# Kernel optimization log

Measured on AMD Instinct MI355X. Metric: run time of the kernel, lower is better.

## Reference

```python
import jax, jax.numpy as jnp
import numpy as np

N, C, K, H = 131072, 256, 32, 8      # points, dim, patch_size, heads
NW = N // K                           # number of windows (4096)
POS_BND = int(0.8 * K)                # 25, as in OctFormer RPE (dilation=1)
RPE_NUM = 2 * POS_BND + 1             # 51


def layer_norm(x, g, b, eps=1e-5):
    m = x.mean(-1, keepdims=True)
    v = jnp.var(x, axis=-1, keepdims=True)
    return (x - m) * jax.lax.rsqrt(v + eps) * g + b


def setup_inputs() -> dict:
    key = jax.random.key(0)
    ks = jax.random.split(key, 12)
    s = 0.02
    return dict(
        data=jax.random.normal(ks[0], (N, C), jnp.float32),
        nbr_idx=jax.random.randint(ks[1], (N, 27), 0, N, dtype=jnp.int32),
        rel_pos=(jax.random.randint(ks[2], (NW, K, K, 3), 0, 2 * K + 1, dtype=jnp.int32) - K),
        patch_mask=jnp.zeros((NW, K, K), jnp.float32),
        w_cpe=jax.random.normal(ks[3], (27, C), jnp.float32) * s,
        bn_g=jnp.ones((C,), jnp.float32), bn_b=jnp.zeros((C,), jnp.float32),
        n1_g=jnp.ones((C,), jnp.float32), n1_b=jnp.zeros((C,), jnp.float32),
        w_qkv=jax.random.normal(ks[4], (C, 3 * C), jnp.float32) * s,
        b_qkv=jnp.zeros((3 * C,), jnp.float32),
        w_proj=jax.random.normal(ks[5], (C, C), jnp.float32) * s,
        b_proj=jnp.zeros((C,), jnp.float32),
        rpe_table=jax.random.normal(ks[6], (3 * RPE_NUM, H), jnp.float32) * s,
        n2_g=jnp.ones((C,), jnp.float32), n2_b=jnp.zeros((C,), jnp.float32),
        w_fc1=jax.random.normal(ks[7], (C, 4 * C), jnp.float32) * s,
        b_fc1=jnp.zeros((4 * C,), jnp.float32),
        w_fc2=jax.random.normal(ks[8], (4 * C, C), jnp.float32) * s,
        b_fc2=jnp.zeros((C,), jnp.float32),
    )


def reference(data, nbr_idx, rel_pos, patch_mask, w_cpe, bn_g, bn_b,
              n1_g, n1_b, w_qkv, b_qkv, w_proj, b_proj, rpe_table,
              n2_g, n2_b, w_fc1, b_fc1, w_fc2, b_fc2):
    # CPE: depthwise 27-neighbor octree conv + eval-mode batchnorm affine
    cpe = jnp.einsum('njc,jc->nc', data[nbr_idx], w_cpe)  # [N,27,C] gather
    data = data + (cpe * bn_g + bn_b)
    # data_to_windows: [N,C] -> [NW,K,C] (N divisible by K)
    x = data.reshape(NW, K, C)

    # windowed attention with inline RPE + additive patch mask
    h = layer_norm(x, n1_g, n1_b)
    qkv = (h @ w_qkv + b_qkv).reshape(NW, K, 3, H, C // H)
    q, k, v = qkv[:, :, 0], qkv[:, :, 1], qkv[:, :, 2]
    scale = (C // H) ** -0.5
    attn = jnp.einsum('nqhd,nkhd->nhqk', q * scale, k)     # [NW,H,K,K]
    idx = jnp.clip(rel_pos, -POS_BND, POS_BND) + POS_BND + jnp.arange(3) * RPE_NUM
    rpe = rpe_table[idx].sum(3)                             # [NW,K,K,H]
    attn = attn + rpe.transpose(0, 3, 1, 2) + patch_mask[:, None]
    attn = jax.nn.softmax(attn, axis=-1)
    out = jnp.einsum('nhqk,nkhd->nqhd', attn, v).reshape(NW, K, C)
    x = x + (out @ w_proj + b_proj)                         # gamma1 = 1

    # MLP (GELU, exact erf like torch default)
    h2 = layer_norm(x, n2_g, n2_b)
    x = x + (jax.nn.gelu(h2 @ w_fc1 + b_fc1, approximate=False) @ w_fc2 + b_fc2)
    return x.reshape(N, C)
```

## Files before the change

kernel.cpp:

```cpp
#include <hip/hip_runtime.h>
#include <stdint.h>


static constexpr int NPT   = 131072;
static constexpr int CC    = 256;
static constexpr int NWIN  = 4096;
static constexpr int NHEAD = 8;

using u16 = unsigned short;
using u32 = unsigned int;
using u8  = unsigned char;

typedef __bf16 bf16x8 __attribute__((ext_vector_type(8)));
typedef float  f32x4  __attribute__((ext_vector_type(4)));
typedef u32    u32x4  __attribute__((ext_vector_type(4)));
typedef u32    u32x2  __attribute__((ext_vector_type(2)));

__device__ __forceinline__ float b2f(u16 u) {
  union { float f; u32 i; } v; v.i = ((u32)u) << 16; return v.f;
}
__device__ __forceinline__ u16 f2b(float f) {
  u32 x = __float_as_uint(f);
  return (u16)((x + 0x7fffu + ((x >> 16) & 1u)) >> 16);
}

__device__ __forceinline__ u8 f2fp8(float f) {
  const u32 s = (__float_as_uint(f) >> 24) & 0x80u;
  float a = fabsf(f);
  if (a >= 0.015625f) {
    u32 b = __float_as_uint(a);
    u32 rb = b + 0x7FFFFu + ((b >> 20) & 1u);
    u32 E = (rb >> 23) - 120u;
    return (u8)(s | (E << 3) | ((rb >> 20) & 7u));
  }
  int k = (int)rintf(a * 512.0f);
  return (u8)(s | (u32)k);
}

template <int J>
__device__ __forceinline__ float fp82f(u32 d) {
#if defined(__has_builtin)
#if __has_builtin(__builtin_amdgcn_cvt_f32_fp8)
  return __builtin_amdgcn_cvt_f32_fp8(d, J);
#else
  const u32 u = (d >> (8 * J)) & 0xFFu;
  const u32 e = (u >> 3) & 15u, m = u & 7u;
  float v = e ? __uint_as_float(((e + 120u) << 23) | (m << 20))
              : (float)m * 0.001953125f;
  return (u & 0x80u) ? -v : v;
#endif
#else
  const u32 u = (d >> (8 * J)) & 0xFFu;
  const u32 e = (u >> 3) & 15u, m = u & 7u;
  float v = e ? __uint_as_float(((e + 120u) << 23) | (m << 20))
              : (float)m * 0.001953125f;
  return (u & 0x80u) ? -v : v;
#endif
}

__device__ __forceinline__ void gload_lds16(const void* g, void* l) {
  using gptr_t = const __attribute__((address_space(1))) uint32_t*;
  using lptr_t = __attribute__((address_space(3))) uint32_t*;
  __builtin_amdgcn_global_load_lds((gptr_t)(uintptr_t)g,
                                   (lptr_t)(uint32_t)(uintptr_t)l, 16, 0, 0);
}

__global__ __launch_bounds__(256) void k_f2b8(const float* __restrict__ in,
                                              u8* __restrict__ out, int n4) {
  for (int i = blockIdx.x * 256 + threadIdx.x; i < n4; i += gridDim.x * 256) {
    float4 v = ((const float4*)in)[i];
    u32 o = (u32)f2fp8(v.x) | ((u32)f2fp8(v.y) << 8) |
            ((u32)f2fp8(v.z) << 16) | ((u32)f2fp8(v.w) << 24);
    ((u32*)out)[i] = o;
  }
}

__global__ __launch_bounds__(256) void k_prep_w(
    const float* __restrict__ wqkv, const float* __restrict__ wproj,
    const float* __restrict__ wfc1, const float* __restrict__ wfc2,
    u16* __restrict__ oqkv, u16* __restrict__ oproj,
    u16* __restrict__ ofc1, u16* __restrict__ ofc2) {
  int i = blockIdx.x * 256 + threadIdx.x;
  if (i < 196608) {
    int c = i >> 8, r = i & 255; oqkv[i] = f2b(wqkv[r * 768 + c]);
  } else if (i < 262144) {
    i -= 196608; int c = i >> 8, r = i & 255; oproj[i] = f2b(wproj[r * 256 + c]);
  } else if (i < 524288) {
    i -= 262144; int c = i >> 8, r = i & 255; ofc1[i] = f2b(wfc1[r * 1024 + c]);
  } else {
    i -= 524288; int c = i >> 10, r = i & 1023; ofc2[i] = f2b(wfc2[r * 256 + c]);
  }
}

__global__ __launch_bounds__(256) void k_cpe_ln1(
    const float* __restrict__ data, const int* __restrict__ nbr,
    const u8* __restrict__ datab, const float* __restrict__ w_cpe,
    const float* __restrict__ bn_g, const float* __restrict__ bn_b,
    const float* __restrict__ n1_g, const float* __restrict__ n1_b,
    float* __restrict__ xo, u16* __restrict__ ho) {
  const int wv   = threadIdx.x >> 6;
  const int lane = threadIdx.x & 63;
  const int n    = blockIdx.x * 4 + wv;
  const int c0   = lane * 4;

  int myidx = 0;
  if (lane < 27) myidx = nbr[n * 27 + lane];

  u32 d[27];
#pragma unroll
  for (int j = 0; j < 27; j++) {
    const int idx = __builtin_amdgcn_readlane(myidx, j);
    d[j] = *(const u32*)(datab + (size_t)idx * CC + c0);
  }

  float a0 = 0.f, a1 = 0.f, a2 = 0.f, a3 = 0.f;
#pragma unroll
  for (int j = 0; j < 27; j++) {
    const float4 wj = *(const float4*)(w_cpe + j * CC + c0);
    a0 += fp82f<0>(d[j]) * wj.x;
    a1 += fp82f<1>(d[j]) * wj.y;
    a2 += fp82f<2>(d[j]) * wj.z;
    a3 += fp82f<3>(d[j]) * wj.w;
  }

  const float4 dv = *(const float4*)(data + (size_t)n * CC + c0);
  const float4 g4 = *(const float4*)(bn_g + c0);
  const float4 b4 = *(const float4*)(bn_b + c0);
  float x0 = dv.x + a0 * g4.x + b4.x;
  float x1 = dv.y + a1 * g4.y + b4.y;
  float x2 = dv.z + a2 * g4.z + b4.z;
  float x3 = dv.w + a3 * g4.w + b4.w;
  *(float4*)(xo + (size_t)n * CC + c0) = make_float4(x0, x1, x2, x3);

  float s  = x0 + x1 + x2 + x3;
  float s2 = x0 * x0 + x1 * x1 + x2 * x2 + x3 * x3;
#pragma unroll
  for (int m = 1; m <= 32; m <<= 1) { s += __shfl_xor(s, m); s2 += __shfl_xor(s2, m); }
  const float mean = s * (1.f / 256.f);
  const float var  = s2 * (1.f / 256.f) - mean * mean;
  const float inv  = rsqrtf(var + 1e-5f);

  const float4 ng = *(const float4*)(n1_g + c0);
  const float4 nb4 = *(const float4*)(n1_b + c0);
  u32x2 o;
  o[0] = (u32)f2b((x0 - mean) * inv * ng.x + nb4.x) |
         ((u32)f2b((x1 - mean) * inv * ng.y + nb4.y) << 16);
  o[1] = (u32)f2b((x2 - mean) * inv * ng.z + nb4.z) |
         ((u32)f2b((x3 - mean) * inv * ng.w + nb4.w) << 16);
  *(u32x2*)(ho + (size_t)n * CC + c0) = o;
}

template <int KD, int ND, int EPI>
__global__ __launch_bounds__(256) void k_gemm(const u16* __restrict__ A,
                                              const u16* __restrict__ Bt,
                                              const float* __restrict__ bias,
                                              u16* __restrict__ outb,
                                              float* __restrict__ outf) {
  __shared__ __align__(16) u16 As[128 * 64];
  __shared__ __align__(16) u16 Bs[128 * 64];
  const int tid = threadIdx.x;
  const int lane = tid & 63;
  const int wv = tid >> 6;
  const int wm = (wv >> 1) * 64;
  const int wn = (wv & 1) * 64;
  const int l15 = lane & 15;
  const int lhi = lane >> 4;

  const int gx = gridDim.x;
  const int bid = blockIdx.y * gx + blockIdx.x;
  const int cpx = (gx * gridDim.y) >> 3;
  const int swz = (bid & 7) * cpx + (bid >> 3);
  const int m0 = (swz / gx) * 128;
  const int n0 = (swz % gx) * 128;

  f32x4 acc[4][4] = {};

  for (int k0 = 0; k0 < KD; k0 += 64) {
#pragma unroll
    for (int i = 0; i < 4; i++) {
      const int off = i * 4096 + tid * 16;
      const int row = off >> 7;
      const int ke  = (off & 127) >> 1;
      gload_lds16(A  + (size_t)(m0 + row) * KD + k0 + ke, (char*)As + off);
      gload_lds16(Bt + (size_t)(n0 + row) * KD + k0 + ke, (char*)Bs + off);
    }
    __syncthreads();
#pragma unroll
    for (int kk = 0; kk < 2; kk++) {
      bf16x8 fa[4], fb[4];
#pragma unroll
      for (int t = 0; t < 4; t++) {
        fa[t] = *(const bf16x8*)&As[(wm + t * 16 + l15) * 64 + kk * 32 + lhi * 8];
        fb[t] = *(const bf16x8*)&Bs[(wn + t * 16 + l15) * 64 + kk * 32 + lhi * 8];
      }
#pragma unroll
      for (int mi = 0; mi < 4; mi++)
#pragma unroll
        for (int ni = 0; ni < 4; ni++)
          acc[mi][ni] = __builtin_amdgcn_mfma_f32_16x16x32_bf16(fa[mi], fb[ni],
                                                                acc[mi][ni], 0, 0, 0);
    }
    __syncthreads();
  }

#pragma unroll
  for (int mi = 0; mi < 4; mi++) {
#pragma unroll
    for (int ni = 0; ni < 4; ni++) {
      const int col = n0 + wn + ni * 16 + l15;
      const float bc = bias[col];
#pragma unroll
      for (int r = 0; r < 4; r++) {
        const int row = m0 + wm + mi * 16 + lhi * 4 + r;
        const size_t o = (size_t)row * ND + col;
        float v = acc[mi][ni][r] + bc;
        if constexpr (EPI == 0) {
          outb[o] = f2b(v);
        } else if constexpr (EPI == 1) {
          outf[o] += v;
        } else {
          v = 0.5f * v * (1.0f + erff(v * 0.70710678118654752f));
          outb[o] = f2b(v);
        }
      }
    }
  }
}

__global__ __launch_bounds__(256) void k_proj_ln2(
    const u16* __restrict__ A, const u16* __restrict__ Bt,
    const float* __restrict__ bias, float* __restrict__ xo,
    const float* __restrict__ n2g, const float* __restrict__ n2b,
    u16* __restrict__ h2) {
  __shared__ __align__(16) u16 As[128 * 64];
  __shared__ __align__(16) u16 Bs[256 * 64];
  const int tid = threadIdx.x;
  const int lane = tid & 63;
  const int wv = tid >> 6;
  const int l15 = lane & 15;
  const int g = lane >> 4;
  const int m0 = blockIdx.x * 128;
  const int wm = wv * 32;

  f32x4 acc[2][16] = {};

  for (int k0 = 0; k0 < 256; k0 += 64) {
#pragma unroll
    for (int i = 0; i < 4; i++) {
      const int off = i * 4096 + tid * 16;
      const int row = off >> 7, ke = (off & 127) >> 1;
      gload_lds16(A + (size_t)(m0 + row) * 256 + k0 + ke, (char*)As + off);
    }
#pragma unroll
    for (int i = 0; i < 8; i++) {
      const int off = i * 4096 + tid * 16;
      const int row = off >> 7, ke = (off & 127) >> 1;
      gload_lds16(Bt + (size_t)row * 256 + k0 + ke, (char*)Bs + off);
    }
    __syncthreads();
#pragma unroll
    for (int kk = 0; kk < 2; kk++) {
      bf16x8 fa[2];
#pragma unroll
      for (int t = 0; t < 2; t++)
        fa[t] = *(const bf16x8*)&As[(wm + t * 16 + l15) * 64 + kk * 32 + g * 8];
#pragma unroll
      for (int ni = 0; ni < 16; ni++) {
        bf16x8 fb = *(const bf16x8*)&Bs[(ni * 16 + l15) * 64 + kk * 32 + g * 8];
#pragma unroll
        for (int mi = 0; mi < 2; mi++)
          acc[mi][ni] = __builtin_amdgcn_mfma_f32_16x16x32_bf16(fa[mi], fb,
                                                                acc[mi][ni], 0, 0, 0);
      }
    }
    __syncthreads();
  }

#pragma unroll
  for (int mi = 0; mi < 2; mi++) {
#pragma unroll
    for (int r = 0; r < 4; r++) {
      const int row = m0 + wm + mi * 16 + g * 4 + r;
      float v[16];
      float s = 0.f, s2 = 0.f;
#pragma unroll
      for (int ni = 0; ni < 16; ni++) {
        const int col = ni * 16 + l15;
        float t = acc[mi][ni][r] + bias[col] + xo[(size_t)row * 256 + col];
        v[ni] = t; s += t; s2 += t * t;
      }
#pragma unroll
      for (int m = 1; m <= 8; m <<= 1) { s += __shfl_xor(s, m); s2 += __shfl_xor(s2, m); }
      const float mean = s * (1.f / 256.f);
      const float var  = s2 * (1.f / 256.f) - mean * mean;
      const float inv  = rsqrtf(var + 1e-5f);
#pragma unroll
      for (int ni = 0; ni < 16; ni++) {
        const int col = ni * 16 + l15;
        xo[(size_t)row * 256 + col] = v[ni];
        h2[(size_t)row * 256 + col] = f2b((v[ni] - mean) * inv * n2g[col] + n2b[col]);
      }
    }
  }
}

__global__ __launch_bounds__(512, 4) void k_attn(const u16* __restrict__ qkv,
                                                 const int* __restrict__ rel_pos,
                                                 const float* __restrict__ pmask,
                                                 const float* __restrict__ rpet,
                                                 u16* __restrict__ out) {
  constexpr int HS = 1288;
  __shared__ __align__(16) u16 smem[24 * HS + 2448];
  u16* sQ = smem;
  u16* sK = smem + 8 * HS;
  u16* sV = smem + 16 * HS;
  float* sT = (float*)(smem + 24 * HS);

  const int tid = threadIdx.x;
  const int nw  = blockIdx.x;
  const int w32 = nw * 32;

  for (int i = tid; i < 1224; i += 512) {
    int h = i / 153, ix = i - h * 153;
    sT[i] = rpet[ix * 8 + h];
  }
#pragma unroll
  for (int j = 0; j < 4; j++) {
    int id  = j * 512 + tid;
    int mat = id >> 10;
    int id1 = id & 1023;
    int h = id1 >> 7, q = (id1 >> 2) & 31, s = id1 & 3;
    u32x4 v = *(const u32x4*)(qkv + (size_t)(w32 + q) * 768 + mat * 256 + h * 32 + s * 8);
    u16* dst = (mat ? sK : sQ) + h * HS + q * 40 + s * 8;
    *(u32x4*)dst = v;
  }
#pragma unroll
  for (int j = 0; j < 2; j++) {
    int id = j * 512 + tid;
    int p = id >> 5, dc = id & 31;
    u32x4 v = *(const u32x4*)(qkv + (size_t)(w32 + p) * 768 + 512 + dc * 8);
    const u16* pv = (const u16*)&v;
#pragma unroll
    for (int jj = 0; jj < 8; jj++) {
      int d = dc * 8 + jj;
      sV[(d >> 5) * HS + (d & 31) * 40 + p] = pv[jj];
    }
  }
  __syncthreads();

  const int h = tid >> 6;
  const int lane = tid & 63;
  const int g = lane >> 4, c = lane & 15;
  const f32x4 zero = {0.f, 0.f, 0.f, 0.f};

  bf16x8 fq[2], fk[2];
#pragma unroll
  for (int t = 0; t < 2; t++) {
    fq[t] = *(const bf16x8*)&sQ[h * HS + (t * 16 + c) * 40 + g * 8];
    fk[t] = *(const bf16x8*)&sK[h * HS + (t * 16 + c) * 40 + g * 8];
  }
  f32x4 S[2][2];
#pragma unroll
  for (int qt = 0; qt < 2; qt++)
#pragma unroll
    for (int kt = 0; kt < 2; kt++)
      S[qt][kt] = __builtin_amdgcn_mfma_f32_16x16x32_bf16(fq[qt], fk[kt], zero, 0, 0, 0);

  const float sc = 0.17677669529663687f;
#pragma unroll
  for (int qt = 0; qt < 2; qt++) {
#pragma unroll
    for (int r = 0; r < 4; r++) {
      const int q = qt * 16 + g * 4 + r;
      const int* rp = rel_pos + ((size_t)(w32 + q) * 32) * 3;
      const float* pm = pmask + (size_t)(w32 + q) * 32;
      float v[2];
#pragma unroll
      for (int kt = 0; kt < 2; kt++) {
        const int k = kt * 16 + c;
        int r0 = rp[k * 3], r1 = rp[k * 3 + 1], r2 = rp[k * 3 + 2];
        r0 = min(max(r0, -25), 25);
        r1 = min(max(r1, -25), 25);
        r2 = min(max(r2, -25), 25);
        const float b = sT[h * 153 + 25 + r0] + sT[h * 153 + 76 + r1] +
                        sT[h * 153 + 127 + r2] + pm[k];
        v[kt] = S[qt][kt][r] * sc + b;
      }
      float m = fmaxf(v[0], v[1]);
#pragma unroll
      for (int d = 1; d <= 8; d <<= 1) m = fmaxf(m, __shfl_xor(m, d));
      const float e0 = __expf(v[0] - m);
      const float e1 = __expf(v[1] - m);
      float ssum = e0 + e1;
#pragma unroll
      for (int d = 1; d <= 8; d <<= 1) ssum += __shfl_xor(ssum, d);
      const float inv = 1.0f / ssum;
      sQ[h * HS + q * 40 + c]      = f2b(e0 * inv);
      sQ[h * HS + q * 40 + 16 + c] = f2b(e1 * inv);
    }
  }
  __builtin_amdgcn_sched_barrier(0);

  bf16x8 fp[2], fv[2];
#pragma unroll
  for (int t = 0; t < 2; t++) {
    fp[t] = *(const bf16x8*)&sQ[h * HS + (t * 16 + c) * 40 + g * 8];
    fv[t] = *(const bf16x8*)&sV[h * HS + (t * 16 + c) * 40 + g * 8];
  }
  f32x4 OT[2][2];
#pragma unroll
  for (int dt = 0; dt < 2; dt++)
#pragma unroll
    for (int qt = 0; qt < 2; qt++)
      OT[dt][qt] = __builtin_amdgcn_mfma_f32_16x16x32_bf16(fv[dt], fp[qt], zero, 0, 0, 0);

  __syncthreads();
  u16* OL = sK;
#pragma unroll
  for (int dt = 0; dt < 2; dt++)
#pragma unroll
    for (int qt = 0; qt < 2; qt++)
#pragma unroll
      for (int r = 0; r < 4; r++) {
        const int d = dt * 16 + g * 4 + r, q = qt * 16 + c;
        OL[q * 264 + h * 32 + d] = f2b(OT[dt][qt][r]);
      }
  __syncthreads();

  {
    const int q = tid >> 4, ch = tid & 15;
    u32x4 w0 = *(const u32x4*)&OL[q * 264 + ch * 16];
    u32x4 w1 = *(const u32x4*)&OL[q * 264 + ch * 16 + 8];
    u16* ob = out + (size_t)(w32 + q) * 256 + ch * 16;
    *(u32x4*)ob = w0;
    *((u32x4*)ob + 1) = w1;
  }
}

extern "C" void kernel_launch(void* const* d_in, const int* in_sizes, int n_in,
                              void* d_out, int out_size, void* d_ws, size_t ws_size,
                              hipStream_t stream) {
  const float* data   = (const float*)d_in[0];
  const int*   nbr    = (const int*)d_in[1];
  const int*   relpos = (const int*)d_in[2];
  const float* pmask  = (const float*)d_in[3];
  const float* w_cpe  = (const float*)d_in[4];
  const float* bn_g   = (const float*)d_in[5];
  const float* bn_b   = (const float*)d_in[6];
  const float* n1_g   = (const float*)d_in[7];
  const float* n1_b   = (const float*)d_in[8];
  const float* w_qkv  = (const float*)d_in[9];
  const float* b_qkv  = (const float*)d_in[10];
  const float* w_proj = (const float*)d_in[11];
  const float* b_proj = (const float*)d_in[12];
  const float* rpet   = (const float*)d_in[13];
  const float* n2_g   = (const float*)d_in[14];
  const float* n2_b   = (const float*)d_in[15];
  const float* w_fc1  = (const float*)d_in[16];
  const float* b_fc1  = (const float*)d_in[17];
  const float* w_fc2  = (const float*)d_in[18];
  const float* b_fc2  = (const float*)d_in[19];
  float* xout = (float*)d_out;

  char* pw = (char*)d_ws;
  u16* buf1 = (u16*)pw; pw += (size_t)NPT * 1024 * 2;
  u16* buf2 = (u16*)pw; pw += (size_t)NPT * 256 * 2;
  u16* wqkvT = (u16*)pw; pw += 768 * 256 * 2;
  u16* wprojT = (u16*)pw; pw += 256 * 256 * 2;
  u16* wfc1T = (u16*)pw; pw += 1024 * 256 * 2;
  u16* wfc2T = (u16*)pw; pw += 256 * 1024 * 2;
  u8* data8 = (u8*)buf1;

  k_f2b8<<<2048, 256, 0, stream>>>(data, data8, NPT * 256 / 4);
  k_prep_w<<<3072, 256, 0, stream>>>(w_qkv, w_proj, w_fc1, w_fc2,
                                     wqkvT, wprojT, wfc1T, wfc2T);

  k_cpe_ln1<<<NPT / 4, 256, 0, stream>>>(data, nbr, data8, w_cpe, bn_g, bn_b, n1_g, n1_b,
                                         xout, buf2);
  k_gemm<256, 768, 0><<<dim3(6, 1024), 256, 0, stream>>>(buf2, wqkvT, b_qkv, buf1, nullptr);
  k_attn<<<NWIN, 512, 0, stream>>>(buf1, relpos, pmask, rpet, buf2);
  k_proj_ln2<<<1024, 256, 0, stream>>>(buf2, wprojT, b_proj, xout, n2_g, n2_b, buf2);
  k_gemm<256, 1024, 2><<<dim3(8, 1024), 256, 0, stream>>>(buf2, wfc1T, b_fc1, buf1, nullptr);
  k_gemm<1024, 256, 1><<<dim3(2, 1024), 256, 0, stream>>>(buf1, wfc2T, b_fc2, nullptr, xout);
}
```

Baseline: 916.3 us.

## Run FC2 GEMM in FP8 and stage CPE weights in shared memory

The FC1 epilogue now writes the GELU activations as FP8 instead of bf16, FC2 weights are converted to FP8, and a new FP8 MFMA GEMM kernel computes FC2. This halves the bytes moved for the largest intermediate and uses the faster FP8 matrix instructions. The CPE/LN1 kernel also loads the depthwise weights into LDS once per block and processes 16 points per block instead of 4, which cuts repeated global weight reads. Both FP8 steps lower the precision of the MLP path.

```diff
diff --git a/kernel.cpp b/kernel.cpp
--- a/kernel.cpp
+++ b/kernel.cpp
@@ -79,7 +79,7 @@
     const float* __restrict__ wqkv, const float* __restrict__ wproj,
     const float* __restrict__ wfc1, const float* __restrict__ wfc2,
     u16* __restrict__ oqkv, u16* __restrict__ oproj,
-    u16* __restrict__ ofc1, u16* __restrict__ ofc2) {
+    u16* __restrict__ ofc1, u8* __restrict__ ofc2) {
   int i = blockIdx.x * 256 + threadIdx.x;
   if (i < 196608) {
     int c = i >> 8, r = i & 255; oqkv[i] = f2b(wqkv[r * 768 + c]);
@@ -88,7 +88,7 @@
   } else if (i < 524288) {
     i -= 262144; int c = i >> 8, r = i & 255; ofc1[i] = f2b(wfc1[r * 1024 + c]);
   } else {
-    i -= 524288; int c = i >> 10, r = i & 1023; ofc2[i] = f2b(wfc2[r * 256 + c]);
+    i -= 524288; int c = i >> 10, r = i & 1023; ofc2[i] = f2fp8(wfc2[r * 256 + c]);
   }
 }
 
@@ -98,56 +98,74 @@
     const float* __restrict__ bn_g, const float* __restrict__ bn_b,
     const float* __restrict__ n1_g, const float* __restrict__ n1_b,
     float* __restrict__ xo, u16* __restrict__ ho) {
-  const int wv   = threadIdx.x >> 6;
-  const int lane = threadIdx.x & 63;
-  const int n    = blockIdx.x * 4 + wv;
+  __shared__ __align__(16) float sW[27 * 256];
+  const int tid = threadIdx.x;
+  {
+    const float4* src = (const float4*)w_cpe;
+    float4* dst = (float4*)sW;
+#pragma unroll
+    for (int i = 0; i < 7; i++) {
+      int idx = i * 256 + tid;
+      if (idx < 27 * 64) dst[idx] = src[idx];
+    }
+  }
+  __syncthreads();
+
+  const int wv   = tid >> 6;
+  const int lane = tid & 63;
   const int c0   = lane * 4;
-
-  int myidx = 0;
-  if (lane < 27) myidx = nbr[n * 27 + lane];
-
-  u32 d[27];
-#pragma unroll
-  for (int j = 0; j < 27; j++) {
-    const int idx = __builtin_amdgcn_readlane(myidx, j);
-    d[j] = *(const u32*)(datab + (size_t)idx * CC + c0);
-  }
-
-  float a0 = 0.f, a1 = 0.f, a2 = 0.f, a3 = 0.f;
-#pragma unroll
-  for (int j = 0; j < 27; j++) {
-    const float4 wj = *(const float4*)(w_cpe + j * CC + c0);
-    a0 += fp82f<0>(d[j]) * wj.x;
-    a1 += fp82f<1>(d[j]) * wj.y;
-    a2 += fp82f<2>(d[j]) * wj.z;
-    a3 += fp82f<3>(d[j]) * wj.w;
-  }
-
-  const float4 dv = *(const float4*)(data + (size_t)n * CC + c0);
-  const float4 g4 = *(const float4*)(bn_g + c0);
-  const float4 b4 = *(const float4*)(bn_b + c0);
-  float x0 = dv.x + a0 * g4.x + b4.x;
-  float x1 = dv.y + a1 * g4.y + b4.y;
-  float x2 = dv.z + a2 * g4.z + b4.z;
-  float x3 = dv.w + a3 * g4.w + b4.w;
-  *(float4*)(xo + (size_t)n * CC + c0) = make_float4(x0, x1, x2, x3);
-
-  float s  = x0 + x1 + x2 + x3;
-  float s2 = x0 * x0 + x1 * x1 + x2 * x2 + x3 * x3;
-#pragma unroll
-  for (int m = 1; m <= 32; m <<= 1) { s += __shfl_xor(s, m); s2 += __shfl_xor(s2, m); }
-  const float mean = s * (1.f / 256.f);
-  const float var  = s2 * (1.f / 256.f) - mean * mean;
-  const float inv  = rsqrtf(var + 1e-5f);
-
-  const float4 ng = *(const float4*)(n1_g + c0);
+  const int n0   = blockIdx.x * 16 + wv * 4;
+
+  const float4 g4  = *(const float4*)(bn_g + c0);
+  const float4 b4  = *(const float4*)(bn_b + c0);
+  const float4 ng  = *(const float4*)(n1_g + c0);
   const float4 nb4 = *(const float4*)(n1_b + c0);
-  u32x2 o;
-  o[0] = (u32)f2b((x0 - mean) * inv * ng.x + nb4.x) |
-         ((u32)f2b((x1 - mean) * inv * ng.y + nb4.y) << 16);
-  o[1] = (u32)f2b((x2 - mean) * inv * ng.z + nb4.z) |
-         ((u32)f2b((x3 - mean) * inv * ng.w + nb4.w) << 16);
-  *(u32x2*)(ho + (size_t)n * CC + c0) = o;
+
+#pragma unroll 1
+  for (int p = 0; p < 4; p++) {
+    const int n = n0 + p;
+    int myidx = 0;
+    if (lane < 27) myidx = nbr[n * 27 + lane];
+
+    u32 d[27];
+#pragma unroll
+    for (int j = 0; j < 27; j++) {
+      const int idx = __builtin_amdgcn_readlane(myidx, j);
+      d[j] = *(const u32*)(datab + (size_t)idx * CC + c0);
+    }
+
+    float a0 = 0.f, a1 = 0.f, a2 = 0.f, a3 = 0.f;
+#pragma unroll
+    for (int j = 0; j < 27; j++) {
+      const float4 wj = *(const float4*)&sW[j * 256 + c0];
+      a0 += fp82f<0>(d[j]) * wj.x;
+      a1 += fp82f<1>(d[j]) * wj.y;
+      a2 += fp82f<2>(d[j]) * wj.z;
+      a3 += fp82f<3>(d[j]) * wj.w;
+    }
+
+    const float4 dv = *(const float4*)(data + (size_t)n * CC + c0);
+    float x0 = dv.x + a0 * g4.x + b4.x;
+    float x1 = dv.y + a1 * g4.y + b4.y;
+    float x2 = dv.z + a2 * g4.z + b4.z;
+    float x3 = dv.w + a3 * g4.w + b4.w;
+    *(float4*)(xo + (size_t)n * CC + c0) = make_float4(x0, x1, x2, x3);
+
+    float s  = x0 + x1 + x2 + x3;
+    float s2 = x0 * x0 + x1 * x1 + x2 * x2 + x3 * x3;
+#pragma unroll
+    for (int m = 1; m <= 32; m <<= 1) { s += __shfl_xor(s, m); s2 += __shfl_xor(s2, m); }
+    const float mean = s * (1.f / 256.f);
+    const float var  = s2 * (1.f / 256.f) - mean * mean;
+    const float inv  = rsqrtf(var + 1e-5f);
+
+    u32x2 o;
+    o[0] = (u32)f2b((x0 - mean) * inv * ng.x + nb4.x) |
+           ((u32)f2b((x1 - mean) * inv * ng.y + nb4.y) << 16);
+    o[1] = (u32)f2b((x2 - mean) * inv * ng.z + nb4.z) |
+           ((u32)f2b((x3 - mean) * inv * ng.w + nb4.w) << 16);
+    *(u32x2*)(ho + (size_t)n * CC + c0) = o;
+  }
 }
 
 template <int KD, int ND, int EPI>
@@ -216,12 +234,76 @@
         float v = acc[mi][ni][r] + bc;
         if constexpr (EPI == 0) {
           outb[o] = f2b(v);
-        } else if constexpr (EPI == 1) {
-          outf[o] += v;
         } else {
           v = 0.5f * v * (1.0f + erff(v * 0.70710678118654752f));
-          outb[o] = f2b(v);
+          ((u8*)outb)[o] = f2fp8(v);
         }
+      }
+    }
+  }
+}
+
+__global__ __launch_bounds__(256) void k_gemm8(const u8* __restrict__ A,
+                                               const u8* __restrict__ Bt,
+                                               const float* __restrict__ bias,
+                                               float* __restrict__ outf) {
+  __shared__ __align__(16) u8 As[128 * 64];
+  __shared__ __align__(16) u8 Bs[128 * 64];
+  const int tid = threadIdx.x;
+  const int lane = tid & 63;
+  const int wv = tid >> 6;
+  const int wm = (wv >> 1) * 64;
+  const int wn = (wv & 1) * 64;
+  const int l15 = lane & 15;
+  const int lhi = lane >> 4;
+
+  const int gx = gridDim.x;
+  const int bid = blockIdx.y * gx + blockIdx.x;
+  const int cpx = (gx * gridDim.y) >> 3;
+  const int swz = (bid & 7) * cpx + (bid >> 3);
+  const int m0 = (swz / gx) * 128;
+  const int n0 = (swz % gx) * 128;
+
+  f32x4 acc[4][4] = {};
+
+  for (int k0 = 0; k0 < 1024; k0 += 64) {
+#pragma unroll
+    for (int i = 0; i < 2; i++) {
+      const int off = i * 4096 + tid * 16;
+      const int row = off >> 6;
+      const int ke  = off & 63;
+      gload_lds16(A  + (size_t)(m0 + row) * 1024 + k0 + ke, (char*)As + off);
+      gload_lds16(Bt + (size_t)(n0 + row) * 1024 + k0 + ke, (char*)Bs + off);
+    }
+    __syncthreads();
+#pragma unroll
+    for (int kk = 0; kk < 2; kk++) {
+      long fa[4], fb[4];
+#pragma unroll
+      for (int t = 0; t < 4; t++) {
+        fa[t] = *(const long*)&As[(wm + t * 16 + l15) * 64 + kk * 32 + lhi * 8];
+        fb[t] = *(const long*)&Bs[(wn + t * 16 + l15) * 64 + kk * 32 + lhi * 8];
+      }
+#pragma unroll
+      for (int mi = 0; mi < 4; mi++)
+#pragma unroll
+        for (int ni = 0; ni < 4; ni++)
+          acc[mi][ni] = __builtin_amdgcn_mfma_f32_16x16x32_fp8_fp8(fa[mi], fb[ni],
+                                                                   acc[mi][ni], 0, 0, 0);
+    }
+    __syncthreads();
+  }
+
+#pragma unroll
+  for (int mi = 0; mi < 4; mi++) {
+#pragma unroll
+    for (int ni = 0; ni < 4; ni++) {
+      const int col = n0 + wn + ni * 16 + l15;
+      const float bc = bias[col];
+#pragma unroll
+      for (int r = 0; r < 4; r++) {
+        const int row = m0 + wm + mi * 16 + lhi * 4 + r;
+        outf[(size_t)row * 256 + col] += acc[mi][ni][r] + bc;
       }
     }
   }
@@ -468,18 +550,18 @@
   u16* wqkvT = (u16*)pw; pw += 768 * 256 * 2;
   u16* wprojT = (u16*)pw; pw += 256 * 256 * 2;
   u16* wfc1T = (u16*)pw; pw += 1024 * 256 * 2;
-  u16* wfc2T = (u16*)pw; pw += 256 * 1024 * 2;
+  u8*  wfc2T8 = (u8*)pw; pw += 256 * 1024;
   u8* data8 = (u8*)buf1;
 
   k_f2b8<<<2048, 256, 0, stream>>>(data, data8, NPT * 256 / 4);
   k_prep_w<<<3072, 256, 0, stream>>>(w_qkv, w_proj, w_fc1, w_fc2,
-                                     wqkvT, wprojT, wfc1T, wfc2T);
-
-  k_cpe_ln1<<<NPT / 4, 256, 0, stream>>>(data, nbr, data8, w_cpe, bn_g, bn_b, n1_g, n1_b,
-                                         xout, buf2);
+                                     wqkvT, wprojT, wfc1T, wfc2T8);
+
+  k_cpe_ln1<<<NPT / 16, 256, 0, stream>>>(data, nbr, data8, w_cpe, bn_g, bn_b,
+                                          n1_g, n1_b, xout, buf2);
   k_gemm<256, 768, 0><<<dim3(6, 1024), 256, 0, stream>>>(buf2, wqkvT, b_qkv, buf1, nullptr);
   k_attn<<<NWIN, 512, 0, stream>>>(buf1, relpos, pmask, rpet, buf2);
   k_proj_ln2<<<1024, 256, 0, stream>>>(buf2, wprojT, b_proj, xout, n2_g, n2_b, buf2);
   k_gemm<256, 1024, 2><<<dim3(8, 1024), 256, 0, stream>>>(buf2, wfc1T, b_fc1, buf1, nullptr);
-  k_gemm<1024, 256, 1><<<dim3(2, 1024), 256, 0, stream>>>(buf1, wfc2T, b_fc2, nullptr, xout);
-}
+  k_gemm8<<<dim3(2, 1024), 256, 0, stream>>>((u8*)buf1, wfc2T8, b_fc2, xout);
+}
```

Result: no change. 918.3 us (+0.2%).
